# Optimization experiments

Hardware: AMD Instinct MI355X
Metric: run time of the kernel (lower is better)

Reference implementation:

```python
import math
import jax, jax.numpy as jnp
import numpy as np


def setup_inputs() -> dict:
    key = jax.random.key(0)
    ks = jax.random.split(key, 9)
    N, e, h = 131072, 512, 8
    s = e // h
    scale = 1.0 / math.sqrt(s)
    return {
        "x": jax.random.normal(ks[0], (N, e), dtype=jnp.float32),
        "Wq": jax.random.normal(ks[1], (h, s, s), dtype=jnp.float32) * scale,
        "bq": jax.random.normal(ks[2], (h, s), dtype=jnp.float32) * 0.01,
        "Wk": jax.random.normal(ks[3], (h, s, s), dtype=jnp.float32) * scale,
        "bk": jax.random.normal(ks[4], (h, s), dtype=jnp.float32) * 0.01,
        "Wv": jax.random.normal(ks[5], (h, s, s), dtype=jnp.float32) * scale,
        "bv": jax.random.normal(ks[6], (h, s), dtype=jnp.float32) * 0.01,
        "Wu": jax.random.normal(ks[7], (e, e), dtype=jnp.float32) * (1.0 / math.sqrt(e)),
        "bu": jax.random.normal(ks[8], (e,), dtype=jnp.float32) * 0.01,
    }


def reference(x, Wq, bq, Wk, bk, Wv, bv, Wu, bu):
    # x: [N, e] features of the N active sparse points; heads h, d_head s = e/h.
    N, e = x.shape
    h = Wq.shape[0]
    s = e // h
    inv_sqrt_e = jnp.float32(1.0 / math.sqrt(e))  # div_t = sqrt(ed)
    xh = x.reshape(N, h, s)
    # Per-head linear maps (batched over heads): [N,h,s] x [h,s,s] -> [N,h,s]
    q = jnp.einsum('nhs,hst->nht', xh, Wq) + bq
    k = jnp.einsum('nhs,hst->nht', xh, Wk) + bk
    v = jnp.einsum('nhs,hst->nht', xh, Wv) + bv
    # Elementwise Q*K, softmax over the feature (d_head) dim, elementwise * V
    a = jax.nn.softmax((q * k) * inv_sqrt_e, axis=-1)
    out = (a * v).reshape(N, e)  # ME.cat over heads == concat along feature dim
    # unifyheads linear
    return out @ Wu + bu
```

## Files before the change

kernel.cpp:

```cpp
#include <hip/hip_runtime.h>


typedef __bf16 bf16x8 __attribute__((ext_vector_type(8)));
typedef float  f32x4  __attribute__((ext_vector_type(4)));

#define MFMA16(A, B, C) __builtin_amdgcn_mfma_f32_16x16x32_bf16((A), (B), (C), 0, 0, 0)

#define NPTS  131072
#define BN    128
#define LDW   88
#define QKSCALE 0.044194173824159216f

__global__ void prep_weights(const float* __restrict__ Wq, const float* __restrict__ Wk,
                             const float* __restrict__ Wv, const float* __restrict__ Wu,
                             __bf16* __restrict__ wu_p, __bf16* __restrict__ wqkv_t)
{
    int idx = blockIdx.x * 512 + threadIdx.x;
    if (idx < 512 * 512) {
        int kk = idx & 63;
        int j  = (idx >> 6) & 511;
        int h  = idx >> 15;
        wu_p[idx] = (__bf16)Wu[(h * 64 + kk) * 512 + j];
    } else {
        int o = idx - 512 * 512;
        if (o < 8 * 192 * 64) {
            int s    = o & 63;
            int row  = (o >> 6) % 192;
            int h    = (o >> 6) / 192;
            int type = row >> 6;
            int t    = row & 63;
            const float* W = (type == 0) ? Wq : (type == 1) ? Wk : Wv;
            wqkv_t[o] = (__bf16)W[h * 4096 + s * 64 + t];
        }
    }
}

__device__ __forceinline__ bf16x8 cvt8(float4 a, float4 b)
{
    bf16x8 r;
    r[0] = (__bf16)a.x; r[1] = (__bf16)a.y; r[2] = (__bf16)a.z; r[3] = (__bf16)a.w;
    r[4] = (__bf16)b.x; r[5] = (__bf16)b.y; r[6] = (__bf16)b.z; r[7] = (__bf16)b.w;
    return r;
}

__global__ __launch_bounds__(512, 2) void fused_attn(
    const float* __restrict__ x,
    const __bf16* __restrict__ wqkv_t,
    const __bf16* __restrict__ wu_p,
    const float* __restrict__ bq, const float* __restrict__ bk,
    const float* __restrict__ bv, const float* __restrict__ bu,
    float* __restrict__ out)
{
    __shared__ __align__(16) __bf16 wu_s[512 * LDW];
    __shared__ __align__(16) __bf16 outs[BN * LDW];

    const int tid  = threadIdx.x;
    const int wave = tid >> 6;
    const int lane = tid & 63;
    const int g    = lane >> 4;
    const int l16  = lane & 15;
    const long n0  = (long)blockIdx.x * BN;

    const int mg = wave & 1;
    const int ng = wave >> 1;

    f32x4 acc[4][8];
    #pragma unroll
    for (int i = 0; i < 4; ++i)
        #pragma unroll
        for (int j = 0; j < 8; ++j)
            acc[i][j] = (f32x4){0.f, 0.f, 0.f, 0.f};

    const float* xrow = x + (n0 + 16 * wave + l16) * 512;

    for (int h = 0; h < 8; ++h) {
        float4 xf0a = *(const float4*)(xrow + h * 64 +  0 + g * 8);
        float4 xf0b = *(const float4*)(xrow + h * 64 +  4 + g * 8);
        float4 xf1a = *(const float4*)(xrow + h * 64 + 32 + g * 8);
        float4 xf1b = *(const float4*)(xrow + h * 64 + 36 + g * 8);

        __syncthreads();

        {
            const uint4* src = (const uint4*)(wu_p + h * 32768);
            const int j = tid >> 3, c = tid & 7;
            #pragma unroll
            for (int p = 0; p < 8; ++p) {
                const int row = j + p * 64;
                uint4 v = src[row * 8 + c];
                *(uint4*)&wu_s[row * LDW + c * 8] = v;
            }
        }

        bf16x8 afr[2];
        afr[0] = cvt8(xf0a, xf0b);
        afr[1] = cvt8(xf1a, xf1b);

        f32x4 qa[4], ka[4], va[4];
        #pragma unroll
        for (int nt = 0; nt < 4; ++nt) {
            qa[nt] = (f32x4){0.f, 0.f, 0.f, 0.f};
            ka[nt] = (f32x4){0.f, 0.f, 0.f, 0.f};
            va[nt] = (f32x4){0.f, 0.f, 0.f, 0.f};
        }
        #pragma unroll
        for (int nt = 0; nt < 4; ++nt) {
            const __bf16* wb = wqkv_t + (h * 192 + nt * 16 + l16) * 64 + g * 8;
            #pragma unroll
            for (int ks = 0; ks < 2; ++ks) {
                qa[nt] = MFMA16(afr[ks], *(const bf16x8*)(wb + ks * 32           ), qa[nt]);
                ka[nt] = MFMA16(afr[ks], *(const bf16x8*)(wb + ks * 32 +  64 * 64), ka[nt]);
                va[nt] = MFMA16(afr[ks], *(const bf16x8*)(wb + ks * 32 + 128 * 64), va[nt]);
            }
        }

        float sum[4] = {0.f, 0.f, 0.f, 0.f};
        float ex[4][4];
        #pragma unroll
        for (int nt = 0; nt < 4; ++nt) {
            const int t = h * 64 + nt * 16 + l16;
            const float bq_ = bq[t], bk_ = bk[t], bv_ = bv[t];
            #pragma unroll
            for (int r = 0; r < 4; ++r) {
                const float qv = qa[nt][r] + bq_;
                const float kv = ka[nt][r] + bk_;
                va[nt][r] += bv_;
                const float e = __expf(qv * kv * QKSCALE);
                ex[nt][r] = e;
                sum[r] += e;
            }
        }
        #pragma unroll
        for (int r = 0; r < 4; ++r) {
            float s = sum[r];
            s += __shfl_xor(s, 1);
            s += __shfl_xor(s, 2);
            s += __shfl_xor(s, 4);
            s += __shfl_xor(s, 8);
            sum[r] = 1.f / s;
        }
        #pragma unroll
        for (int nt = 0; nt < 4; ++nt)
            #pragma unroll
            for (int r = 0; r < 4; ++r) {
                const float o = ex[nt][r] * sum[r] * va[nt][r];
                outs[(16 * wave + 4 * g + r) * LDW + nt * 16 + l16] = (__bf16)o;
            }

        __syncthreads();

        #pragma unroll
        for (int ks = 0; ks < 2; ++ks) {
            bf16x8 afc[4], bfc[8];
            #pragma unroll
            for (int m = 0; m < 4; ++m)
                afc[m] = *(const bf16x8*)&outs[(mg * 64 + m * 16 + l16) * LDW + ks * 32 + g * 8];
            #pragma unroll
            for (int n = 0; n < 8; ++n)
                bfc[n] = *(const bf16x8*)&wu_s[(ng * 128 + n * 16 + l16) * LDW + ks * 32 + g * 8];
            #pragma unroll
            for (int m = 0; m < 4; ++m)
                #pragma unroll
                for (int n = 0; n < 8; ++n)
                    acc[m][n] = MFMA16(afc[m], bfc[n], acc[m][n]);
        }
    }

    #pragma unroll
    for (int n = 0; n < 8; ++n) {
        const int col = ng * 128 + n * 16 + l16;
        const float bu_ = bu[col];
        #pragma unroll
        for (int m = 0; m < 4; ++m) {
            const long rowbase = (n0 + mg * 64 + m * 16 + 4 * g) * 512;
            #pragma unroll
            for (int r = 0; r < 4; ++r)
                out[rowbase + (long)r * 512 + col] = acc[m][n][r] + bu_;
        }
    }
}

extern "C" void kernel_launch(void* const* d_in, const int* in_sizes, int n_in,
                              void* d_out, int out_size, void* d_ws, size_t ws_size,
                              hipStream_t stream)
{
    const float* x  = (const float*)d_in[0];
    const float* Wq = (const float*)d_in[1];
    const float* bq = (const float*)d_in[2];
    const float* Wk = (const float*)d_in[3];
    const float* bk = (const float*)d_in[4];
    const float* Wv = (const float*)d_in[5];
    const float* bv = (const float*)d_in[6];
    const float* Wu = (const float*)d_in[7];
    const float* bu = (const float*)d_in[8];
    float* out = (float*)d_out;

    __bf16* wu_p   = (__bf16*)d_ws;
    __bf16* wqkv_t = (__bf16*)((char*)d_ws + 512 * 512 * 2);

    prep_weights<<<704, 512, 0, stream>>>(Wq, Wk, Wv, Wu, wu_p, wqkv_t);
    fused_attn<<<NPTS / BN, 512, 0, stream>>>(x, wqkv_t, wu_p, bq, bk, bv, bu, out);
}
```

Baseline: 735.8 us.

## Split fused attention into attn kernel plus separate bf16 GEMM via workspace

Replaces the single fused kernel with two kernels when the workspace is large enough. The first computes the per-head QKV, softmax and V product, prefetches the next head's x, and writes a bf16 attention tensor to the workspace. The second is a tiled 128x128 GEMM that uses global_load_lds to stage tiles and adds the bias. The aim is to drop the fused kernel's large per-block LDS reload of Wu and its low occupancy, at the cost of an extra 128 MB round trip through global memory.

```diff
diff --git a/kernel.cpp b/kernel.cpp
--- a/kernel.cpp
+++ b/kernel.cpp
@@ -7,9 +7,225 @@
 #define MFMA16(A, B, C) __builtin_amdgcn_mfma_f32_16x16x32_bf16((A), (B), (C), 0, 0, 0)
 
 #define NPTS  131072
+#define QKSCALE 0.044194173824159216f
+
+__device__ __forceinline__ bf16x8 cvt8(float4 a, float4 b)
+{
+    bf16x8 r;
+    r[0] = (__bf16)a.x; r[1] = (__bf16)a.y; r[2] = (__bf16)a.z; r[3] = (__bf16)a.w;
+    r[4] = (__bf16)b.x; r[5] = (__bf16)b.y; r[6] = (__bf16)b.z; r[7] = (__bf16)b.w;
+    return r;
+}
+
+__device__ __forceinline__ void gload_lds16(const void* g, void* lds)
+{
+    __builtin_amdgcn_global_load_lds(
+        (const __attribute__((address_space(1))) unsigned int*)g,
+        (__attribute__((address_space(3))) unsigned int*)lds, 16, 0, 0);
+}
+
+
+__global__ void prep_split(const float* __restrict__ Wq, const float* __restrict__ Wk,
+                           const float* __restrict__ Wv, const float* __restrict__ Wu,
+                           __bf16* __restrict__ wqkv_t, __bf16* __restrict__ wu_t)
+{
+    int idx = blockIdx.x * 256 + threadIdx.x;
+    if (idx < 512 * 512) {
+        int n = idx >> 9, k = idx & 511;
+        wu_t[idx] = (__bf16)Wu[k * 512 + n];
+    } else {
+        int o = idx - 512 * 512;
+        if (o < 8 * 192 * 64) {
+            int s    = o & 63;
+            int row  = (o >> 6) % 192;
+            int hh   = (o >> 6) / 192;
+            int type = row >> 6;
+            int t    = row & 63;
+            const float* W = (type == 0) ? Wq : (type == 1) ? Wk : Wv;
+            wqkv_t[o] = (__bf16)W[hh * 4096 + s * 64 + t];
+        }
+    }
+}
+
+#define ALD 72
+__global__ __launch_bounds__(256, 4) void attn_kernel(
+    const float* __restrict__ x,
+    const __bf16* __restrict__ wqkv_t,
+    const float* __restrict__ bq, const float* __restrict__ bk,
+    const float* __restrict__ bv,
+    __bf16* __restrict__ attn)
+{
+    __shared__ __align__(16) __bf16 slab[4][16 * ALD];
+
+    const int tid  = threadIdx.x;
+    const int wave = tid >> 6;
+    const int lane = tid & 63;
+    const int g    = lane >> 4;
+    const int l16  = lane & 15;
+    const long row0 = (long)blockIdx.x * 64 + wave * 16;
+
+    const float* xrow = x + (row0 + l16) * 512;
+    __bf16* wslab = &slab[wave][0];
+
+    float4 xa = *(const float4*)(xrow +  0 + g * 8);
+    float4 xb = *(const float4*)(xrow +  4 + g * 8);
+    float4 xc = *(const float4*)(xrow + 32 + g * 8);
+    float4 xd = *(const float4*)(xrow + 36 + g * 8);
+
+    for (int h = 0; h < 8; ++h) {
+        bf16x8 a0 = cvt8(xa, xb);
+        bf16x8 a1 = cvt8(xc, xd);
+        if (h < 7) {
+            const float* xn = xrow + (h + 1) * 64;
+            xa = *(const float4*)(xn +  0 + g * 8);
+            xb = *(const float4*)(xn +  4 + g * 8);
+            xc = *(const float4*)(xn + 32 + g * 8);
+            xd = *(const float4*)(xn + 36 + g * 8);
+        }
+
+        f32x4 qa[4], ka[4], va[4];
+        #pragma unroll
+        for (int nt = 0; nt < 4; ++nt) {
+            qa[nt] = (f32x4){0.f, 0.f, 0.f, 0.f};
+            ka[nt] = (f32x4){0.f, 0.f, 0.f, 0.f};
+            va[nt] = (f32x4){0.f, 0.f, 0.f, 0.f};
+        }
+        #pragma unroll
+        for (int nt = 0; nt < 4; ++nt) {
+            const __bf16* wb = wqkv_t + (h * 192 + nt * 16 + l16) * 64 + g * 8;
+            #pragma unroll
+            for (int ks = 0; ks < 2; ++ks) {
+                const bf16x8 af = ks ? a1 : a0;
+                qa[nt] = MFMA16(af, *(const bf16x8*)(wb + ks * 32           ), qa[nt]);
+                ka[nt] = MFMA16(af, *(const bf16x8*)(wb + ks * 32 +  64 * 64), ka[nt]);
+                va[nt] = MFMA16(af, *(const bf16x8*)(wb + ks * 32 + 128 * 64), va[nt]);
+            }
+        }
+
+        float sum[4] = {0.f, 0.f, 0.f, 0.f};
+        float ex[4][4];
+        #pragma unroll
+        for (int nt = 0; nt < 4; ++nt) {
+            const int t = h * 64 + nt * 16 + l16;
+            const float bq_ = bq[t], bk_ = bk[t], bv_ = bv[t];
+            #pragma unroll
+            for (int r = 0; r < 4; ++r) {
+                const float qv = qa[nt][r] + bq_;
+                const float kv = ka[nt][r] + bk_;
+                va[nt][r] += bv_;
+                const float e = __expf(qv * kv * QKSCALE);
+                ex[nt][r] = e;
+                sum[r] += e;
+            }
+        }
+        #pragma unroll
+        for (int r = 0; r < 4; ++r) {
+            float s = sum[r];
+            s += __shfl_xor(s, 1);
+            s += __shfl_xor(s, 2);
+            s += __shfl_xor(s, 4);
+            s += __shfl_xor(s, 8);
+            sum[r] = 1.f / s;
+        }
+
+        #pragma unroll
+        for (int nt = 0; nt < 4; ++nt)
+            #pragma unroll
+            for (int r = 0; r < 4; ++r)
+                wslab[(4 * g + r) * ALD + nt * 16 + l16] =
+                    (__bf16)(ex[nt][r] * sum[r] * va[nt][r]);
+
+        __builtin_amdgcn_s_waitcnt(0xc07f);
+
+        #pragma unroll
+        for (int p = 0; p < 2; ++p) {
+            const int row = p * 8 + (lane >> 3);
+            const int c   = lane & 7;
+            uint4 v = *(const uint4*)&wslab[row * ALD + c * 8];
+            *(uint4*)&attn[(row0 + row) * 512 + h * 64 + c * 8] = v;
+        }
+    }
+}
+
+#define BM 128
+#define BNC 128
+#define BK 64
+__global__ __launch_bounds__(256, 3) void gemm_kernel(
+    const __bf16* __restrict__ attn,
+    const __bf16* __restrict__ wu_t,
+    const float* __restrict__ bu,
+    float* __restrict__ out)
+{
+    __shared__ __align__(16) __bf16 As[BM * BK];
+    __shared__ __align__(16) __bf16 Bs[BNC * BK];
+
+    const int tid  = threadIdx.x;
+    const int wave = tid >> 6;
+    const int lane = tid & 63;
+    const int g    = lane >> 4;
+    const int l16  = lane & 15;
+    const int mw   = wave & 1;
+    const int nw   = wave >> 1;
+
+    const long m0 = (long)blockIdx.y * BM;
+    const int  n0 = blockIdx.x * BNC;
+
+    f32x4 acc[4][4];
+    #pragma unroll
+    for (int m = 0; m < 4; ++m)
+        #pragma unroll
+        for (int n = 0; n < 4; ++n)
+            acc[m][n] = (f32x4){0.f, 0.f, 0.f, 0.f};
+
+    const int srow  = tid >> 3;
+    const int schnk = tid & 7;
+
+    for (int k0 = 0; k0 < 512; k0 += BK) {
+        __syncthreads();
+        #pragma unroll
+        for (int p = 0; p < 4; ++p) {
+            const int row = p * 32 + srow;
+            gload_lds16(attn + (m0 + row) * 512 + k0 + schnk * 8,
+                        (char*)As + p * 4096 + tid * 16);
+            gload_lds16(wu_t + (long)(n0 + row) * 512 + k0 + schnk * 8,
+                        (char*)Bs + p * 4096 + tid * 16);
+        }
+        __syncthreads();
+
+        #pragma unroll
+        for (int ks = 0; ks < 2; ++ks) {
+            bf16x8 af[4], bf[4];
+            #pragma unroll
+            for (int m = 0; m < 4; ++m)
+                af[m] = *(const bf16x8*)&As[(mw * 64 + m * 16 + l16) * BK + ks * 32 + g * 8];
+            #pragma unroll
+            for (int n = 0; n < 4; ++n)
+                bf[n] = *(const bf16x8*)&Bs[(nw * 64 + n * 16 + l16) * BK + ks * 32 + g * 8];
+            #pragma unroll
+            for (int m = 0; m < 4; ++m)
+                #pragma unroll
+                for (int n = 0; n < 4; ++n)
+                    acc[m][n] = MFMA16(af[m], bf[n], acc[m][n]);
+        }
+    }
+
+    #pragma unroll
+    for (int n = 0; n < 4; ++n) {
+        const int col = n0 + nw * 64 + n * 16 + l16;
+        const float bu_ = bu[col];
+        #pragma unroll
+        for (int m = 0; m < 4; ++m) {
+            const long rowb = m0 + mw * 64 + m * 16 + 4 * g;
+            #pragma unroll
+            for (int r = 0; r < 4; ++r)
+                out[(rowb + r) * 512 + col] = acc[m][n][r] + bu_;
+        }
+    }
+}
+
+
 #define BN    128
 #define LDW   88
-#define QKSCALE 0.044194173824159216f
 
 __global__ void prep_weights(const float* __restrict__ Wq, const float* __restrict__ Wk,
                              const float* __restrict__ Wv, const float* __restrict__ Wu,
@@ -35,14 +251,6 @@
     }
 }
 
-__device__ __forceinline__ bf16x8 cvt8(float4 a, float4 b)
-{
-    bf16x8 r;
-    r[0] = (__bf16)a.x; r[1] = (__bf16)a.y; r[2] = (__bf16)a.z; r[3] = (__bf16)a.w;
-    r[4] = (__bf16)b.x; r[5] = (__bf16)b.y; r[6] = (__bf16)b.z; r[7] = (__bf16)b.w;
-    return r;
-}
-
 __global__ __launch_bounds__(512, 2) void fused_attn(
     const float* __restrict__ x,
     const __bf16* __restrict__ wqkv_t,
@@ -195,9 +403,21 @@
     const float* bu = (const float*)d_in[8];
     float* out = (float*)d_out;
 
-    __bf16* wu_p   = (__bf16*)d_ws;
-    __bf16* wqkv_t = (__bf16*)((char*)d_ws + 512 * 512 * 2);
-
-    prep_weights<<<704, 512, 0, stream>>>(Wq, Wk, Wv, Wu, wu_p, wqkv_t);
-    fused_attn<<<NPTS / BN, 512, 0, stream>>>(x, wqkv_t, wu_p, bq, bk, bv, bu, out);
-}
+    const size_t attn_bytes = (size_t)NPTS * 512 * 2;
+    const size_t need = attn_bytes + 196608 + 524288;
+
+    if (ws_size >= need) {
+        __bf16* attn   = (__bf16*)d_ws;
+        __bf16* wqkv_t = (__bf16*)((char*)d_ws + attn_bytes);
+        __bf16* wu_t   = (__bf16*)((char*)d_ws + attn_bytes + 196608);
+
+        prep_split<<<1408, 256, 0, stream>>>(Wq, Wk, Wv, Wu, wqkv_t, wu_t);
+        attn_kernel<<<NPTS / 64, 256, 0, stream>>>(x, wqkv_t, bq, bk, bv, attn);
+        gemm_kernel<<<dim3(4, NPTS / BM), 256, 0, stream>>>(attn, wu_t, bu, out);
+    } else {
+        __bf16* wu_p   = (__bf16*)d_ws;
+        __bf16* wqkv_t = (__bf16*)((char*)d_ws + 512 * 512 * 2);
+        prep_weights<<<704, 512, 0, stream>>>(Wq, Wk, Wv, Wu, wu_p, wqkv_t);
+        fused_attn<<<NPTS / BN, 512, 0, stream>>>(x, wqkv_t, wu_p, bq, bk, bv, bu, out);
+    }
+}
```

Result: faster. 706.1 us (-4.0%).
